# Kernel optimization log

Measured on AMD Instinct MI355X. Metric: run time of the kernel, lower is better.

Reference implementation:

```python
import jax, jax.numpy as jnp
import numpy as np

WORD_THRES = 0.2
COS_EPS = 1e-8
NEG_INF = -1e9


def setup_inputs() -> dict:
    key = jax.random.key(0)
    k1, k2, k3, k4 = jax.random.split(key, 4)
    B, L, V, E, A = 1024, 256, 50000, 300, 30
    inputs = jax.random.randint(k1, (B, L), 0, V)            # token ids, 0 == pad
    w_emb = jax.random.normal(k2, (V, E), dtype=jnp.float32) * 0.1
    a_emb = jax.random.normal(k3, (A, E), dtype=jnp.float32)
    a_weight = jax.random.uniform(k4, (A,), dtype=jnp.float32)
    return {"inputs": inputs, "w_emb": w_emb, "a_emb": a_emb, "a_weight": a_weight}


def reference(inputs, w_emb, a_emb, a_weight):
    # inputs: [B, L] int ids; w_emb: [V, E]; a_emb: [A, E]; a_weight: [A]
    inputs_len = (inputs != 0).sum(axis=1).astype(jnp.float32)      # [B]
    x_wrd = w_emb[inputs]                                            # [B, L, E]

    # cosine similarity between each aspect and each word (torch semantics:
    # dot / (max(||a||, eps) * max(||x||, eps)))
    a_norm = jnp.maximum(jnp.linalg.norm(a_emb, axis=-1), COS_EPS)   # [A]
    x_norm = jnp.maximum(jnp.linalg.norm(x_wrd, axis=-1), COS_EPS)   # [B, L]
    dot = jnp.einsum("ae,ble->abl", a_emb, x_wrd)                    # [A, B, L]
    sim = dot / (a_norm[:, None, None] * x_norm[None, :, :])

    # Threshold(word_thres, 0): x if x > thres else 0, then scale by aspect weight
    sim = jnp.where(sim > WORD_THRES, sim, 0.0) * a_weight[:, None, None]

    # centroid score: relu(sim).max over aspects, summed over seq, length-normalized
    centroid = jnp.maximum(sim, 0.0).max(axis=0)                     # [B, L]
    centroid_score = centroid.sum(axis=1) / (inputs_len + 1e-5)      # [B]

    # attention: mask exact zeros to -1e9, max over aspects, softmax over seq
    sim_m = jnp.where(sim == 0.0, NEG_INF, sim)
    scores = sim_m.max(axis=0)                                       # [B, L]
    a = jax.nn.softmax(scores, axis=1)                               # [B, L]

    z = jnp.einsum("bl,ble->be", a, x_wrd)                           # [B, E]
    enc_out = z * (centroid_score > 1e-4).astype(z.dtype)[:, None]
    return enc_out, a, centroid_score
```

## Files before the change

### kernel.cpp

```cpp
#include <hip/hip_runtime.h>
#include <math.h>

#define BB 1024
#define LL 256
#define VV 50000
#define EE 300
#define AA 30
#define WORD_THRES 0.2f
#define COS_EPS_F 1e-8f
#define NEG_INF_F -1e9f
#define RECHECK_DELTA 2e-4f

typedef __attribute__((ext_vector_type(8))) short bf16x8;
typedef __attribute__((ext_vector_type(4))) float f32x4;

#define MFMA16(a, b, c) __builtin_amdgcn_mfma_f32_16x16x32_bf16((a), (b), (c), 0, 0, 0)

__device__ __forceinline__ unsigned pack_hi(float a, float b) {
    return (__float_as_uint(a) >> 16) | (__float_as_uint(b) & 0xFFFF0000u);
}
__device__ __forceinline__ float hi_part(float a) {
    return __uint_as_float(__float_as_uint(a) & 0xFFFF0000u);
}
__device__ __forceinline__ void cvt_hilo(const float4 f0, const float4 f1,
                                         uint4& uh, uint4& ul) {
    uh.x = pack_hi(f0.x, f0.y);
    uh.y = pack_hi(f0.z, f0.w);
    uh.z = pack_hi(f1.x, f1.y);
    uh.w = pack_hi(f1.z, f1.w);
    const float l0 = f0.x - hi_part(f0.x), l1 = f0.y - hi_part(f0.y);
    const float l2 = f0.z - hi_part(f0.z), l3 = f0.w - hi_part(f0.w);
    const float l4 = f1.x - hi_part(f1.x), l5 = f1.y - hi_part(f1.y);
    const float l6 = f1.z - hi_part(f1.z), l7 = f1.w - hi_part(f1.w);
    ul.x = pack_hi(l0, l1);
    ul.y = pack_hi(l2, l3);
    ul.z = pack_hi(l4, l5);
    ul.w = pack_hi(l6, l7);
}

__device__ __forceinline__ void ld_pair(const float* __restrict__ rowp, int kb,
                                        float4& a, float4& b) {
    const int k0 = (kb > 296) ? 296 : kb;
    const int k1 = (kb + 4 > 296) ? 296 : (kb + 4);
    a = *(const float4*)(rowp + k0);
    b = *(const float4*)(rowp + k1);
}

__global__ void __launch_bounds__(256) cent_kernel(
    const float* __restrict__ w_emb,
    const float* __restrict__ a_emb,
    const float* __restrict__ a_weight,
    float* __restrict__ cent)
{
    __shared__ uint4 s_bfrag[40 * 64];
    __shared__ float s_scale[32];
    __shared__ float s_aw[32];

    const int t = threadIdx.x;
    const int l = t & 63;
    const int w = t >> 6;
    const int m = l & 15;
    const int kg = l >> 4;

    {
        const int a = t >> 3, j = t & 7;
        if (a < AA) {
            const float4* a4 = (const float4*)a_emb + a * 75;
            float n2a = 0.f;
            for (int c = j; c < 75; c += 8) {
                const float4 x = a4[c];
                n2a += x.x * x.x + x.y * x.y + x.z * x.z + x.w * x.w;
            }
            n2a += __shfl_xor(n2a, 1);
            n2a += __shfl_xor(n2a, 2);
            n2a += __shfl_xor(n2a, 4);
            if (j == 0) {
                s_scale[a] = 1.f / fmaxf(sqrtf(n2a), COS_EPS_F);
                s_aw[a] = a_weight[a];
            }
        }
        if (t == 30 || t == 31) { s_scale[t] = 0.f; s_aw[t] = 0.f; }
    }

    for (int ks = w; ks < 10; ks += 4) {
        const int kb = kg * 8 + 32 * ks;
#pragma unroll
        for (int tt = 0; tt < 2; ++tt) {
            const int col = tt * 16 + m;
            float4 f0 = {0.f, 0.f, 0.f, 0.f}, f1 = {0.f, 0.f, 0.f, 0.f};
            if (col < AA) {
                const float* ap = a_emb + col * EE;
                if (kb <= 296) f0 = *(const float4*)(ap + kb);
                if (kb <= 292) f1 = *(const float4*)(ap + kb + 4);
            }
            uint4 uh, ul;
            cvt_hilo(f0, f1, uh, ul);
            s_bfrag[(ks * 4 + tt * 2 + 0) * 64 + l] = uh;
            s_bfrag[(ks * 4 + tt * 2 + 1) * 64 + l] = ul;
        }
    }
    __syncthreads();

    const int vbase = blockIdx.x * 64 + w * 16;
    const int v = vbase + m;
    const float* __restrict__ rowp = w_emb + (size_t)((v < VV) ? v : 0) * EE;

    f32x4 acc0 = {0.f, 0.f, 0.f, 0.f};
    f32x4 acc1 = {0.f, 0.f, 0.f, 0.f};
    float n2 = 0.f;
    const uint4* __restrict__ bp0 = s_bfrag + l;

    float4 pa[5], pb[5];
#pragma unroll
    for (int i = 0; i < 5; ++i)
        ld_pair(rowp, kg * 8 + 32 * i, pa[i], pb[i]);

#pragma unroll
    for (int i = 0; i < 10; ++i) {
        const int s = i % 5;
        float4 f0 = pa[s], f1 = pb[s];
        if (i < 5)
            ld_pair(rowp, kg * 8 + 32 * (i + 5), pa[s], pb[s]);
        if (i == 9) {
            const float4 z = {0.f, 0.f, 0.f, 0.f};
            if (kg >= 2) f0 = z;
            if (kg >= 1) f1 = z;
        }
        n2 = fmaf(f0.x, f0.x, fmaf(f0.y, f0.y, fmaf(f0.z, f0.z, fmaf(f0.w, f0.w, n2))));
        n2 = fmaf(f1.x, f1.x, fmaf(f1.y, f1.y, fmaf(f1.z, f1.z, fmaf(f1.w, f1.w, n2))));
        uint4 uh, ul;
        cvt_hilo(f0, f1, uh, ul);
        const bf16x8 ah = __builtin_bit_cast(bf16x8, uh);
        const bf16x8 al = __builtin_bit_cast(bf16x8, ul);
        const uint4* bp = bp0 + i * 256;
        const bf16x8 bh0 = __builtin_bit_cast(bf16x8, bp[0]);
        const bf16x8 bl0 = __builtin_bit_cast(bf16x8, bp[64]);
        const bf16x8 bh1 = __builtin_bit_cast(bf16x8, bp[128]);
        const bf16x8 bl1 = __builtin_bit_cast(bf16x8, bp[192]);
        acc0 = MFMA16(ah, bh0, acc0);
        acc1 = MFMA16(ah, bh1, acc1);
        acc0 = MFMA16(ah, bl0, acc0);
        acc1 = MFMA16(ah, bl1, acc1);
        acc0 = MFMA16(al, bh0, acc0);
        acc1 = MFMA16(al, bh1, acc1);
    }

    n2 += __shfl_xor(n2, 16);
    n2 += __shfl_xor(n2, 32);

    const float sc0 = s_scale[m], aw0 = s_aw[m];
    const float sc1 = s_scale[16 + m], aw1 = s_aw[16 + m];
    const bool col1ok = (16 + m) < AA;
    float mx[4];
#pragma unroll
    for (int j = 0; j < 4; ++j) {
        const int r = kg * 4 + j;
        const float n2r = __int_as_float(
            __builtin_amdgcn_ds_bpermute(r << 2, __float_as_int(n2)));
        const float inv_x = 1.f / fmaxf(sqrtf(n2r), COS_EPS_F);
        float c0 = acc0[j] * sc0 * inv_x;
        float c1 = acc1[j] * sc1 * inv_x;
        if (fabsf(c0 - WORD_THRES) < RECHECK_DELTA) {
            const int rr = vbase + r;
            const float* wr = w_emb + (size_t)((rr < VV) ? rr : 0) * EE;
            const float* ar = a_emb + m * EE;
            float d = 0.f;
            for (int k = 0; k < EE; ++k) d = fmaf(wr[k], ar[k], d);
            c0 = d * sc0 * inv_x;
        }
        if (col1ok && fabsf(c1 - WORD_THRES) < RECHECK_DELTA) {
            const int rr = vbase + r;
            const float* wr = w_emb + (size_t)((rr < VV) ? rr : 0) * EE;
            const float* ar = a_emb + (16 + m) * EE;
            float d = 0.f;
            for (int k = 0; k < EE; ++k) d = fmaf(wr[k], ar[k], d);
            c1 = d * sc1 * inv_x;
        }
        float mj = fmaxf((c0 > WORD_THRES) ? c0 * aw0 : 0.f,
                         (c1 > WORD_THRES) ? c1 * aw1 : 0.f);
        mj = fmaxf(mj, __shfl_xor(mj, 1));
        mj = fmaxf(mj, __shfl_xor(mj, 2));
        mj = fmaxf(mj, __shfl_xor(mj, 4));
        mj = fmaxf(mj, __shfl_xor(mj, 8));
        mx[j] = mj;
    }
    if (m == 0 && vbase < VV) {
        const float4 o = {mx[0], mx[1], mx[2], mx[3]};
        *(float4*)(cent + vbase + kg * 4) = o;
    }
}

__global__ void __launch_bounds__(256) row_kernel(
    const int* __restrict__ inputs,
    const float* __restrict__ w_emb,
    const float* __restrict__ cent,
    float* __restrict__ out)
{
    const int w = threadIdx.x >> 6;
    const int lane = threadIdx.x & 63;
    const int b = blockIdx.x * 4 + w;

    __shared__ int s_id[4][LL];
    __shared__ float s_w[4][LL];
    __shared__ int s_n[4];

    if (lane == 0) s_n[w] = 0;

    const int4 id4 = *(const int4*)(inputs + b * LL + lane * 4);
    const float c0 = cent[id4.x];
    const float c1 = cent[id4.y];
    const float c2 = cent[id4.z];
    const float c3 = cent[id4.w];
    const float sc0 = (c0 > 0.f) ? c0 : NEG_INF_F;
    const float sc1 = (c1 > 0.f) ? c1 : NEG_INF_F;
    const float sc2 = (c2 > 0.f) ? c2 : NEG_INF_F;
    const float sc3 = (c3 > 0.f) ? c3 : NEG_INF_F;

    float s1 = c0 + c1 + c2 + c3;
    float s2 = (id4.x != 0 ? 1.f : 0.f) + (id4.y != 0 ? 1.f : 0.f) +
               (id4.z != 0 ? 1.f : 0.f) + (id4.w != 0 ? 1.f : 0.f);
    float s3 = fmaxf(fmaxf(sc0, sc1), fmaxf(sc2, sc3));
#pragma unroll
    for (int o = 1; o < 64; o <<= 1) {
        s1 += __shfl_xor(s1, o);
        s2 += __shfl_xor(s2, o);
        s3 = fmaxf(s3, __shfl_xor(s3, o));
    }
    const float mx = s3;

    const float p0 = expf(sc0 - mx);
    const float p1 = expf(sc1 - mx);
    const float p2 = expf(sc2 - mx);
    const float p3 = expf(sc3 - mx);
    float s4 = p0 + p1 + p2 + p3;
#pragma unroll
    for (int o = 1; o < 64; o <<= 1) s4 += __shfl_xor(s4, o);

    const float rinv = 1.f / s4;
    const float4 av = {p0 * rinv, p1 * rinv, p2 * rinv, p3 * rinv};
    *(float4*)(out + BB * EE + b * LL + lane * 4) = av;

    const float cs = s1 / (s2 + 1e-5f);
    const float gate = (cs > 1e-4f) ? 1.f : 0.f;
    if (lane == 0) out[BB * EE + BB * LL + b] = cs;

    if (sc0 > -1e8f) { const int i = atomicAdd(&s_n[w], 1); s_id[w][i] = id4.x; s_w[w][i] = av.x; }
    if (sc1 > -1e8f) { const int i = atomicAdd(&s_n[w], 1); s_id[w][i] = id4.y; s_w[w][i] = av.y; }
    if (sc2 > -1e8f) { const int i = atomicAdd(&s_n[w], 1); s_id[w][i] = id4.z; s_w[w][i] = av.z; }
    if (sc3 > -1e8f) { const int i = atomicAdd(&s_n[w], 1); s_id[w][i] = id4.w; s_w[w][i] = av.w; }
    __syncthreads();
    const int n = s_n[w];

    float4 accA = {0.f, 0.f, 0.f, 0.f};
    float4 accB = {0.f, 0.f, 0.f, 0.f};
    for (int i = 0; i < n; ++i) {
        const float wgt = s_w[w][i];
        const float4* rp = (const float4*)(w_emb + (size_t)s_id[w][i] * EE);
        const float4 ra = rp[lane];
        accA.x += wgt * ra.x; accA.y += wgt * ra.y;
        accA.z += wgt * ra.z; accA.w += wgt * ra.w;
        if (lane < 11) {
            const float4 rb = rp[64 + lane];
            accB.x += wgt * rb.x; accB.y += wgt * rb.y;
            accB.z += wgt * rb.z; accB.w += wgt * rb.w;
        }
    }
    accA.x *= gate; accA.y *= gate; accA.z *= gate; accA.w *= gate;
    *(float4*)(out + b * EE + 4 * lane) = accA;
    if (lane < 11) {
        accB.x *= gate; accB.y *= gate; accB.z *= gate; accB.w *= gate;
        *(float4*)(out + b * EE + 256 + 4 * lane) = accB;
    }
}

extern "C" void kernel_launch(void* const* d_in, const int* in_sizes, int n_in,
                              void* d_out, int out_size, void* d_ws, size_t ws_size,
                              hipStream_t stream) {
    const int* inputs = (const int*)d_in[0];
    const float* w_emb = (const float*)d_in[1];
    const float* a_emb = (const float*)d_in[2];
    const float* a_weight = (const float*)d_in[3];
    float* out = (float*)d_out;
    float* cent = (float*)d_ws;

    cent_kernel<<<(VV + 63) / 64, 256, 0, stream>>>(w_emb, a_emb, a_weight, cent);
    row_kernel<<<BB / 4, 256, 0, stream>>>(inputs, w_emb, cent, out);
}
```

Before: 111.6 us.

## Stage vocab embedding rows into LDS via direct global-to-LDS loads in cent_kernel

The cent kernel now copies each block's 32 contiguous w_emb rows into shared memory with coalesced global_load_lds 16-byte transfers, replacing strided per-lane register prefetches. It then reads its MFMA fragments and the recheck rows from LDS. Blocks shrink to 128 threads and 32 rows, doubling the grid, and the aspect-norm and B-fragment setup loops are adjusted to fit. This adds about 38KB of LDS per block, which limits occupancy, and puts a full vmcnt wait before compute, so the load is no longer overlapped with MFMA work inside a block.

```diff
diff --git a/kernel.cpp b/kernel.cpp
--- a/kernel.cpp
+++ b/kernel.cpp
@@ -15,6 +15,12 @@
 typedef __attribute__((ext_vector_type(4))) float f32x4;
 
 #define MFMA16(a, b, c) __builtin_amdgcn_mfma_f32_16x16x32_bf16((a), (b), (c), 0, 0, 0)
+
+__device__ __forceinline__ void gld_lds16(const float* g, float* l) {
+    typedef const __attribute__((address_space(1))) void* gas_p;
+    typedef __attribute__((address_space(3))) void* las_p;
+    __builtin_amdgcn_global_load_lds((gas_p)g, (las_p)l, 16, 0, 0);
+}
 
 __device__ __forceinline__ unsigned pack_hi(float a, float b) {
     return (__float_as_uint(a) >> 16) | (__float_as_uint(b) & 0xFFFF0000u);
@@ -38,20 +44,13 @@
     ul.w = pack_hi(l6, l7);
 }
 
-__device__ __forceinline__ void ld_pair(const float* __restrict__ rowp, int kb,
-                                        float4& a, float4& b) {
-    const int k0 = (kb > 296) ? 296 : kb;
-    const int k1 = (kb + 4 > 296) ? 296 : (kb + 4);
-    a = *(const float4*)(rowp + k0);
-    b = *(const float4*)(rowp + k1);
-}
-
-__global__ void __launch_bounds__(256) cent_kernel(
+__global__ void __launch_bounds__(128) cent_kernel(
     const float* __restrict__ w_emb,
     const float* __restrict__ a_emb,
     const float* __restrict__ a_weight,
     float* __restrict__ cent)
 {
+    __shared__ float4 s_a4[2400];
     __shared__ uint4 s_bfrag[40 * 64];
     __shared__ float s_scale[32];
     __shared__ float s_aw[32];
@@ -61,19 +60,33 @@
     const int w = t >> 6;
     const int m = l & 15;
     const int kg = l >> 4;
+    float* s_af = (float*)s_a4;
 
     {
-        const int a = t >> 3, j = t & 7;
+        const float* gbase = w_emb + (size_t)blockIdx.x * 32 * EE;
+        const float* gend = w_emb + (size_t)VV * EE;
+#pragma unroll
+        for (int i = 0; i < 19; ++i) {
+            if (i < 18 || t < 96) {
+                const int off = i * 512 + t * 4;
+                const float* src = gbase + off;
+                if (src > gend - 4) src = gend - 4;
+                gld_lds16(src, s_af + off);
+            }
+        }
+    }
+
+    {
+        const int a = t >> 2, j = t & 3;
         if (a < AA) {
             const float4* a4 = (const float4*)a_emb + a * 75;
             float n2a = 0.f;
-            for (int c = j; c < 75; c += 8) {
+            for (int c = j; c < 75; c += 4) {
                 const float4 x = a4[c];
                 n2a += x.x * x.x + x.y * x.y + x.z * x.z + x.w * x.w;
             }
             n2a += __shfl_xor(n2a, 1);
             n2a += __shfl_xor(n2a, 2);
-            n2a += __shfl_xor(n2a, 4);
             if (j == 0) {
                 s_scale[a] = 1.f / fmaxf(sqrtf(n2a), COS_EPS_F);
                 s_aw[a] = a_weight[a];
@@ -82,7 +95,7 @@
         if (t == 30 || t == 31) { s_scale[t] = 0.f; s_aw[t] = 0.f; }
     }
 
-    for (int ks = w; ks < 10; ks += 4) {
+    for (int ks = w; ks < 10; ks += 2) {
         const int kb = kg * 8 + 32 * ks;
 #pragma unroll
         for (int tt = 0; tt < 2; ++tt) {
@@ -99,28 +112,23 @@
             s_bfrag[(ks * 4 + tt * 2 + 1) * 64 + l] = ul;
         }
     }
+
+    asm volatile("s_waitcnt vmcnt(0)" ::: "memory");
     __syncthreads();
 
-    const int vbase = blockIdx.x * 64 + w * 16;
-    const int v = vbase + m;
-    const float* __restrict__ rowp = w_emb + (size_t)((v < VV) ? v : 0) * EE;
+    const int vtile = blockIdx.x * 32 + w * 16;
+    const float* __restrict__ arow = s_af + (w * 16 + m) * EE;
 
     f32x4 acc0 = {0.f, 0.f, 0.f, 0.f};
     f32x4 acc1 = {0.f, 0.f, 0.f, 0.f};
     float n2 = 0.f;
     const uint4* __restrict__ bp0 = s_bfrag + l;
 
-    float4 pa[5], pb[5];
-#pragma unroll
-    for (int i = 0; i < 5; ++i)
-        ld_pair(rowp, kg * 8 + 32 * i, pa[i], pb[i]);
-
 #pragma unroll
     for (int i = 0; i < 10; ++i) {
-        const int s = i % 5;
-        float4 f0 = pa[s], f1 = pb[s];
-        if (i < 5)
-            ld_pair(rowp, kg * 8 + 32 * (i + 5), pa[s], pb[s]);
+        const int kb = kg * 8 + 32 * i;
+        float4 f0 = *(const float4*)(arow + kb);
+        float4 f1 = *(const float4*)(arow + kb + 4);
         if (i == 9) {
             const float4 z = {0.f, 0.f, 0.f, 0.f};
             if (kg >= 2) f0 = z;
@@ -161,16 +169,14 @@
         float c0 = acc0[j] * sc0 * inv_x;
         float c1 = acc1[j] * sc1 * inv_x;
         if (fabsf(c0 - WORD_THRES) < RECHECK_DELTA) {
-            const int rr = vbase + r;
-            const float* wr = w_emb + (size_t)((rr < VV) ? rr : 0) * EE;
+            const float* wr = s_af + (w * 16 + r) * EE;
             const float* ar = a_emb + m * EE;
             float d = 0.f;
             for (int k = 0; k < EE; ++k) d = fmaf(wr[k], ar[k], d);
             c0 = d * sc0 * inv_x;
         }
         if (col1ok && fabsf(c1 - WORD_THRES) < RECHECK_DELTA) {
-            const int rr = vbase + r;
-            const float* wr = w_emb + (size_t)((rr < VV) ? rr : 0) * EE;
+            const float* wr = s_af + (w * 16 + r) * EE;
             const float* ar = a_emb + (16 + m) * EE;
             float d = 0.f;
             for (int k = 0; k < EE; ++k) d = fmaf(wr[k], ar[k], d);
@@ -184,9 +190,9 @@
         mj = fmaxf(mj, __shfl_xor(mj, 8));
         mx[j] = mj;
     }
-    if (m == 0 && vbase < VV) {
+    if (m == 0 && vtile < VV) {
         const float4 o = {mx[0], mx[1], mx[2], mx[3]};
-        *(float4*)(cent + vbase + kg * 4) = o;
+        *(float4*)(cent + vtile + kg * 4) = o;
     }
 }
 
@@ -283,6 +289,6 @@
     float* out = (float*)d_out;
     float* cent = (float*)d_ws;
 
-    cent_kernel<<<(VV + 63) / 64, 256, 0, stream>>>(w_emb, a_emb, a_weight, cent);
+    cent_kernel<<<(VV + 31) / 32, 128, 0, stream>>>(w_emb, a_emb, a_weight, cent);
     row_kernel<<<BB / 4, 256, 0, stream>>>(inputs, w_emb, cent, out);
 }
```

New measurement: 135.8 us. +21.6%, slower.
